# Optimization experiments

Measured on AMD Instinct MI355X. Metric: run time of the kernel, lower is better.

## Reference

```python
import jax, jax.numpy as jnp
import numpy as np

D_MODEL = 1024
D_STATE = 16
LN_EPS = 1e-5


def setup_inputs() -> dict:
    key = jax.random.key(0)
    ks = jax.random.split(key, 10)
    B, T = 8, 4096
    s = 1.0 / np.sqrt(D_MODEL)
    inp = {
        "x": jax.random.normal(ks[0], (B, T, D_MODEL), jnp.float32),
        "h0": jnp.zeros((B, D_STATE), jnp.float32),
        "mask": jnp.ones((B, T), jnp.float32),
        # params
        "A_diag": -jnp.abs(jax.random.normal(ks[1], (D_STATE,), jnp.float32) * 0.01),
        "W_delta": jax.random.uniform(ks[2], (D_STATE, D_MODEL), jnp.float32, -s, s),
        "W_B": jax.random.uniform(ks[3], (D_STATE, D_MODEL), jnp.float32, -s, s),
        "W_C": jax.random.uniform(ks[4], (D_STATE, D_MODEL), jnp.float32, -s, s),
        "W_out": jax.random.uniform(ks[5], (D_MODEL, D_STATE), jnp.float32, -1/np.sqrt(D_STATE), 1/np.sqrt(D_STATE)),
        "D": jnp.ones((D_MODEL,), jnp.float32),
        "W_gate": jax.random.uniform(ks[6], (D_MODEL, D_MODEL), jnp.float32, -s, s),
        "b_gate": jax.random.uniform(ks[7], (D_MODEL,), jnp.float32, -s, s),
        "ln_w": jnp.ones((D_MODEL,), jnp.float32),
        "ln_b": jnp.zeros((D_MODEL,), jnp.float32),
    }
    return inp


def _layernorm(x, w, b):
    mu = jnp.mean(x, axis=-1, keepdims=True)
    var = jnp.var(x, axis=-1, keepdims=True)
    return (x - mu) * jax.lax.rsqrt(var + LN_EPS) * w + b


def reference(x, h0, mask, A_diag, W_delta, W_B, W_C, W_out, D, W_gate, b_gate, ln_w, ln_b):
    # Per-step projections depend only on x_t -> vectorize over T up front.
    gate = jax.nn.sigmoid(_layernorm(jnp.einsum('btd,ed->bte', x, W_gate) + b_gate, ln_w, ln_b))
    xg = gate * x                                        # [B,T,d_model]
    delta = jax.nn.softplus(jnp.einsum('btd,sd->bts', xg, W_delta))
    Bt = jnp.einsum('btd,sd->bts', xg, W_B)              # [B,T,d_state]
    Ct = jnp.einsum('btd,sd->bts', xg, W_C)
    A_bar = jnp.exp(delta * A_diag)                      # [B,T,d_state]
    m = mask[..., None]                                  # [B,T,1]

    def step(h, inputs):
        a_t, b_t, m_t = inputs                           # [B,ds],[B,ds],[B,1]
        h_cand = jnp.tanh(a_t * h + b_t)
        h_new = h_cand * m_t + h * (1.0 - m_t)
        return h_new, h_new

    # scan over time: move T to leading axis
    h_final, hs = jax.lax.scan(
        step, h0,
        (jnp.swapaxes(A_bar, 0, 1), jnp.swapaxes(Bt, 0, 1), jnp.swapaxes(m, 0, 1)))
    hs = jnp.swapaxes(hs, 0, 1)                          # [B,T,d_state]
    s = Ct * hs
    y = jnp.einsum('bts,ds->btd', s, W_out) + D * x      # [B,T,d_model]
    return (y, h_final)
```

## Files before the change

kernel.cpp:

```cpp
#include <hip/hip_runtime.h>
#include <hip/hip_bf16.h>
#include <cstdint>

#define M_TOK   32768
#define LNEPS   1e-5f
#define TWO_LOG2E 2.8853900817779268f

typedef float  f32x4 __attribute__((ext_vector_type(4)));
typedef short  s16x8 __attribute__((ext_vector_type(8)));

__device__ __forceinline__ unsigned short f2b(float v) {
  return __builtin_bit_cast(unsigned short, __float2bfloat16(v));
}
__device__ __forceinline__ float b2f(unsigned short u) {
  return __bfloat162float(__builtin_bit_cast(__hip_bfloat16, u));
}

__device__ __forceinline__ void async_cp16(const void* g, void* l) {
  using gp = const __attribute__((address_space(1))) char*;
  using lp = __attribute__((address_space(3))) char*;
  __builtin_amdgcn_global_load_lds((gp)(uint64_t)g,
                                   (lp)(uint32_t)(uint64_t)l, 16, 0, 0);
}

__global__ __launch_bounds__(256) void k_convert(
    const float* __restrict__ x, const float* __restrict__ wg,
    const float* __restrict__ wd, const float* __restrict__ wb,
    const float* __restrict__ wc,
    unsigned short* __restrict__ Xb, unsigned short* __restrict__ Wgb,
    unsigned short* __restrict__ Wcat) {
  int i = blockIdx.x * 256 + threadIdx.x;
  const float* src;
  unsigned short* dst;
  if (i < 8388608) {
    src = x + (size_t)i * 4; dst = Xb + (size_t)i * 4;
  } else if (i < 8650752) {
    int j = i - 8388608;
    src = wg + (size_t)j * 4; dst = Wgb + (size_t)j * 4;
  } else {
    int j = i - 8650752;
    int e = j * 4;
    if (e < 16384)       src = wd + e;
    else if (e < 32768)  src = wb + (e - 16384);
    else                 src = wc + (e - 32768);
    dst = Wcat + e;
  }
  float4 v = *(const float4*)src;
  ushort4 o;
  o.x = f2b(v.x); o.y = f2b(v.y); o.z = f2b(v.z); o.w = f2b(v.w);
  *(ushort4*)dst = o;
}

__global__ __launch_bounds__(256, 2) void k_gemm_gate(
    const unsigned short* __restrict__ A,
    const unsigned short* __restrict__ Bm,
    unsigned short* __restrict__ C) {
  __shared__ unsigned short As[128 * 32];
  __shared__ unsigned short Bs[128 * 32];
  const int tid  = threadIdx.x;
  const int wave = tid >> 6, lane = tid & 63;
  const int wr = wave >> 1, wc = wave & 1;
  const int lrow = lane & 15, lq = lane >> 4;
  const int lin  = blockIdx.y * gridDim.x + blockIdx.x;
  const int unit = (lin & 7) * 256 + (lin >> 3);
  const int m0 = (unit >> 3) * 128;
  const int n0 = (unit & 7) * 128;
  const int crow  = tid >> 2;
  const int ccol  = (tid & 3) * 8;

  f32x4 acc[4][4];
#pragma unroll
  for (int i = 0; i < 4; i++)
#pragma unroll
    for (int j = 0; j < 4; j++) acc[i][j] = (f32x4){0.f, 0.f, 0.f, 0.f};

  for (int k0 = 0; k0 < 1024; k0 += 32) {
    async_cp16(A + (size_t)(m0 + crow) * 1024 + k0 + ccol,
               (void*)(As + (wave * 64) * 8));
    async_cp16(A + (size_t)(m0 + crow + 64) * 1024 + k0 + ccol,
               (void*)(As + (256 + wave * 64) * 8));
    async_cp16(Bm + (size_t)(n0 + crow) * 1024 + k0 + ccol,
               (void*)(Bs + (wave * 64) * 8));
    async_cp16(Bm + (size_t)(n0 + crow + 64) * 1024 + k0 + ccol,
               (void*)(Bs + (256 + wave * 64) * 8));
    __syncthreads();

    s16x8 af[4], bfr[4];
#pragma unroll
    for (int i = 0; i < 4; i++)
      af[i] = *(const s16x8*)(As + (wr * 64 + i * 16 + lrow) * 32 + lq * 8);
#pragma unroll
    for (int j = 0; j < 4; j++)
      bfr[j] = *(const s16x8*)(Bs + (wc * 64 + j * 16 + lrow) * 32 + lq * 8);
#pragma unroll
    for (int i = 0; i < 4; i++)
#pragma unroll
      for (int j = 0; j < 4; j++)
        acc[i][j] = __builtin_amdgcn_mfma_f32_16x16x32_bf16(
            af[i], bfr[j], acc[i][j], 0, 0, 0);
    __syncthreads();
  }

#pragma unroll
  for (int i = 0; i < 4; i++)
#pragma unroll
    for (int j = 0; j < 4; j++)
#pragma unroll
      for (int r = 0; r < 4; r++) {
        int row = m0 + wr * 64 + i * 16 + lq * 4 + r;
        int col = n0 + wc * 64 + j * 16 + lrow;
        C[(size_t)row * 1024 + col] = f2b(acc[i][j][r]);
      }
}

__global__ __launch_bounds__(256) void k_lngate(
    const unsigned short* Gin, const float* __restrict__ x,
    const float* __restrict__ bg, const float* __restrict__ lnw,
    const float* __restrict__ lnb, unsigned short* XG) {
  __shared__ float red[8];
  const int t = threadIdx.x;
  const size_t r = blockIdx.x;
  const int e = t * 4;

  ushort4 g4 = *(const ushort4*)(Gin + r * 1024 + e);
  float4 bg4 = *(const float4*)(bg + e);
  float v0 = b2f(g4.x) + bg4.x;
  float v1 = b2f(g4.y) + bg4.y;
  float v2 = b2f(g4.z) + bg4.z;
  float v3 = b2f(g4.w) + bg4.w;

  float s  = v0 + v1 + v2 + v3;
  float ss = v0 * v0 + v1 * v1 + v2 * v2 + v3 * v3;
#pragma unroll
  for (int off = 32; off >= 1; off >>= 1) {
    s  += __shfl_xor(s, off, 64);
    ss += __shfl_xor(ss, off, 64);
  }
  if ((t & 63) == 0) { red[t >> 6] = s; red[4 + (t >> 6)] = ss; }
  __syncthreads();
  float tot = red[0] + red[1] + red[2] + red[3];
  float tss = red[4] + red[5] + red[6] + red[7];
  float mu  = tot * (1.0f / 1024.0f);
  float var = tss * (1.0f / 1024.0f) - mu * mu;
  float rs  = rsqrtf(var + LNEPS);

  float4 xv = *(const float4*)(x + r * 1024 + e);
  float4 w4 = *(const float4*)(lnw + e);
  float4 b4 = *(const float4*)(lnb + e);
  float u0 = (v0 - mu) * rs * w4.x + b4.x;
  float u1 = (v1 - mu) * rs * w4.y + b4.y;
  float u2 = (v2 - mu) * rs * w4.z + b4.z;
  float u3 = (v3 - mu) * rs * w4.w + b4.w;
  float g0 = 1.0f / (1.0f + __expf(-u0));
  float g1 = 1.0f / (1.0f + __expf(-u1));
  float g2 = 1.0f / (1.0f + __expf(-u2));
  float g3 = 1.0f / (1.0f + __expf(-u3));
  ushort4 o;
  o.x = f2b(g0 * xv.x); o.y = f2b(g1 * xv.y);
  o.z = f2b(g2 * xv.z); o.w = f2b(g3 * xv.w);
  *(ushort4*)(XG + r * 1024 + e) = o;
}

__global__ __launch_bounds__(256) void k_proj(
    const unsigned short* __restrict__ XG, const unsigned short* __restrict__ Wcat,
    const float* __restrict__ A_diag,
    float* __restrict__ UV, float* __restrict__ Ct, int* __restrict__ flags) {
  __shared__ unsigned short As[64 * 32];
  __shared__ unsigned short Bs[48 * 32];
  const int tid  = threadIdx.x;
  const int wave = tid >> 6, lane = tid & 63;
  const int lrow = lane & 15, lq = lane >> 4;
  const int r0 = blockIdx.x * 64;
  const int crow = tid >> 2, ccol = (tid & 3) * 8;

  if (blockIdx.x == 0 && tid < 8)
    __hip_atomic_store(&flags[tid], 0, __ATOMIC_RELAXED,
                       __HIP_MEMORY_SCOPE_AGENT);

  f32x4 acc[3];
#pragma unroll
  for (int j = 0; j < 3; j++) acc[j] = (f32x4){0.f, 0.f, 0.f, 0.f};

  for (int k0 = 0; k0 < 1024; k0 += 32) {
    uint4 av = *(const uint4*)(XG + (size_t)(r0 + crow) * 1024 + k0 + ccol);
    uint4 bv;
    if (tid < 192) bv = *(const uint4*)(Wcat + (size_t)crow * 1024 + k0 + ccol);
    __syncthreads();
    *(uint4*)(As + crow * 32 + ccol) = av;
    if (tid < 192) *(uint4*)(Bs + crow * 32 + ccol) = bv;
    __syncthreads();
    s16x8 af = *(const s16x8*)(As + (wave * 16 + lrow) * 32 + lq * 8);
#pragma unroll
    for (int j = 0; j < 3; j++) {
      s16x8 bf8 = *(const s16x8*)(Bs + (j * 16 + lrow) * 32 + lq * 8);
      acc[j] = __builtin_amdgcn_mfma_f32_16x16x32_bf16(af, bf8, acc[j], 0, 0, 0);
    }
  }

  float ad = A_diag[lrow];
#pragma unroll
  for (int r = 0; r < 4; r++) {
    int row = r0 + wave * 16 + lq * 4 + r;
    float z  = acc[0][r];
    float sp = fmaxf(z, 0.0f) + log1pf(__expf(-fabsf(z)));
    float A2 = __expf(sp * ad) * TWO_LOG2E;
    float B2 = acc[1][r] * TWO_LOG2E;
    float2 o;
    o.x = A2 + B2;
    o.y = -2.0f * A2;
    *(float2*)(UV + (size_t)row * 32 + lrow * 2) = o;
    Ct[(size_t)row * 16 + lrow] = acc[2][r];
  }
}

#define TC 128
#define NCH (4096 / TC)
#define NOUT 512

__device__ __forceinline__ void load16(float2 (&P)[16], const float* uvb,
                                       int j, int lane) {
#pragma unroll
  for (int i = 0; i < 16; ++i)
    P[i] = *(const float2*)(uvb + ((j * 16 + i) * 16 + lane) * 2);
}
__device__ __forceinline__ void fast16(float2 (&P)[16], float& r, float& h,
                                       float* hhb, int j, int lane) {
#pragma unroll
  for (int i = 0; i < 16; ++i) {
    float w = fmaf(P[i].y, r, P[i].x);
    float e = __builtin_amdgcn_exp2f(w);
    r = __builtin_amdgcn_rcpf(e + 1.0f);
    h = fmaf(-2.0f, r, 1.0f);
    hhb[(j * 16 + i) * 16 + lane] = h;
  }
}
__device__ __forceinline__ void slow16(float2 (&P)[16], float& h,
                                       const float* mb, float* hhb,
                                       int j, int lane) {
#pragma unroll
  for (int i = 0; i < 16; ++i) {
    float v  = P[i].y, u = P[i].x;
    float A2 = -0.5f * v;
    float B2 = fmaf(0.5f, v, u);
    float w  = fmaf(A2, h, B2);
    float e  = __builtin_amdgcn_exp2f(w);
    float rr = __builtin_amdgcn_rcpf(e + 1.0f);
    float th = fmaf(-2.0f, rr, 1.0f);
    float m  = mb[j * 16 + i];
    h = fmaf(m, th - h, h);
    hhb[(j * 16 + i) * 16 + lane] = h;
  }
}

__global__ __launch_bounds__(512, 6) void k_scan_out(
    const float* __restrict__ UV, const float* __restrict__ mask,
    const float* __restrict__ h0, float* __restrict__ hs,
    float* __restrict__ hfin,
    const float* __restrict__ Ct, const float* __restrict__ x,
    const float* __restrict__ Wout, const float* __restrict__ Dd,
    float* __restrict__ y, int* __restrict__ flags) {
  __shared__ float uvL[2][TC * 32];
  __shared__ float hhL[2][TC * 16];
  __shared__ float mskL[2][TC];

  const int tid = threadIdx.x;

  if (blockIdx.x >= 8) {
    const int o    = blockIdx.x - 8;
    const int wv   = tid >> 6;
    const int lane = tid & 63;
    const int d0   = wv * 128 + lane * 2;
    const int b0   = o >> 7;
    const int b1   = b0 + 4;
    const int j0   = o & 127;

    float wa[16], wb[16];
#pragma unroll
    for (int q = 0; q < 4; q++) {
      *(float4*)&wa[q * 4] = *(const float4*)(Wout + (size_t)d0 * 16 + q * 4);
      *(float4*)&wb[q * 4] = *(const float4*)(Wout + (size_t)(d0 + 1) * 16 + q * 4);
    }
    float2 D2 = *(const float2*)(Dd + d0);

    for (int c = 0; c < NCH; ++c) {
      size_t r0 = (size_t)b0 * 4096 + (size_t)c * TC + j0;
      size_t r1 = (size_t)b1 * 4096 + (size_t)c * TC + j0;
      int spins = 0;
      for (;;) {
        int f = 0;
        if (lane == 0) {
          int fa = __hip_atomic_load(&flags[b0], __ATOMIC_RELAXED,
                                     __HIP_MEMORY_SCOPE_AGENT);
          int fb = __hip_atomic_load(&flags[b1], __ATOMIC_RELAXED,
                                     __HIP_MEMORY_SCOPE_AGENT);
          f = (fa < fb) ? fa : fb;
        }
        f = __shfl(f, 0);
        if (f > c || spins > (1 << 18)) break;
        ++spins;
        __builtin_amdgcn_s_sleep(32);
      }
      float cv0 = Ct[r0 * 16 + (lane & 15)];
      float cv1 = Ct[r1 * 16 + (lane & 15)];
      float hv0 = __hip_atomic_load(&hs[r0 * 16 + (lane & 15)],
                                    __ATOMIC_RELAXED, __HIP_MEMORY_SCOPE_AGENT);
      float hv1 = __hip_atomic_load(&hs[r1 * 16 + (lane & 15)],
                                    __ATOMIC_RELAXED, __HIP_MEMORY_SCOPE_AGENT);
      float2 x20 = *(const float2*)(x + r0 * 1024 + d0);
      float2 x21 = *(const float2*)(x + r1 * 1024 + d0);
      float sv0 = cv0 * hv0;
      float sv1 = cv1 * hv1;
      float a0x = D2.x * x20.x, a0y = D2.y * x20.y;
      float a1x = D2.x * x21.x, a1y = D2.y * x21.y;
#pragma unroll
      for (int s = 0; s < 16; s++) {
        float s0 = __shfl(sv0, s);
        float s1 = __shfl(sv1, s);
        a0x = fmaf(wa[s], s0, a0x);
        a0y = fmaf(wb[s], s0, a0y);
        a1x = fmaf(wa[s], s1, a1x);
        a1y = fmaf(wb[s], s1, a1y);
      }
      float2 o0; o0.x = a0x; o0.y = a0y;
      float2 o1; o1.x = a1x; o1.y = a1y;
      *(float2*)(y + r0 * 1024 + d0) = o0;
      *(float2*)(y + r1 * 1024 + d0) = o1;
    }
    return;
  }

  const int b   = blockIdx.x;
  const float* pm = mask + (size_t)b * 4096;
  const size_t uvbase = (size_t)b * 4096 * 32;
  const size_t hsbase = (size_t)b * 4096 * 16;

  if (tid < 64) __builtin_amdgcn_s_setprio(3);

  float h = 0.f, r = 0.f;
  if (tid < 16) {
    h = h0[b * 16 + tid];
    r = 0.5f - 0.5f * h;
  }

  if (tid >= 64) {
    int pt = tid - 64;
    const uint4* src = (const uint4*)(UV + uvbase);
    for (int i = pt; i < TC * 8; i += 448) ((uint4*)uvL[0])[i] = src[i];
    if (tid < 128) {
      int l = tid - 64;
      mskL[0][l]      = pm[l];
      mskL[0][l + 64] = pm[l + 64];
    }
  }
  __syncthreads();

  for (int c = 0; c < NCH; ++c) {
    if (c >= 2 && tid == 511) {
      __hip_atomic_store(&flags[b], c - 1, __ATOMIC_RELAXED,
                         __HIP_MEMORY_SCOPE_AGENT);
    }
    const int p = c & 1;
    if (tid < 64) {
      const int lane = tid;
      float mv0 = mskL[p][2 * lane], mv1 = mskL[p][2 * lane + 1];
      bool on = (mv0 == 1.0f) && (mv1 == 1.0f);
      bool allones = (__ballot(on) == 0xFFFFFFFFFFFFFFFFull);
      if (lane < 16) {
        const float* uvb = uvL[p];
        float* hhb = hhL[p];
        float2 Pa[16], Pb[16];
        load16(Pa, uvb, 0, lane);
        if (allones) {
#pragma unroll
          for (int j = 0; j < 8; j += 2) {
            load16(Pb, uvb, j + 1, lane);
            fast16(Pa, r, h, hhb, j, lane);
            if (j + 2 < 8) load16(Pa, uvb, j + 2, lane);
            fast16(Pb, r, h, hhb, j + 1, lane);
          }
        } else {
#pragma unroll
          for (int j = 0; j < 8; j += 2) {
            load16(Pb, uvb, j + 1, lane);
            slow16(Pa, h, mskL[p], hhb, j, lane);
            if (j + 2 < 8) load16(Pa, uvb, j + 2, lane);
            slow16(Pb, h, mskL[p], hhb, j + 1, lane);
          }
          r = 0.5f - 0.5f * h;
        }
      }
    } else {
      int pt = tid - 64;
      if (c + 1 < NCH) {
        const uint4* src =
            (const uint4*)(UV + uvbase + (size_t)(c + 1) * TC * 32);
        uint4* dst = (uint4*)uvL[(c + 1) & 1];
        for (int i = pt; i < TC * 8; i += 448) dst[i] = src[i];
        if (tid < 128) {
          int l = tid - 64;
          mskL[(c + 1) & 1][l]      = pm[(c + 1) * TC + l];
          mskL[(c + 1) & 1][l + 64] = pm[(c + 1) * TC + l + 64];
        }
      }
      if (c > 0) {
        const unsigned long long* s2 = (const unsigned long long*)hhL[(c - 1) & 1];
        unsigned long long* d2 =
            (unsigned long long*)(hs + hsbase + (size_t)(c - 1) * TC * 16);
        for (int i = pt; i < TC * 8; i += 448)
          __hip_atomic_store(&d2[i], s2[i], __ATOMIC_RELAXED,
                             __HIP_MEMORY_SCOPE_AGENT);
      }
    }
    __syncthreads();
  }

  {
    const unsigned long long* s2 = (const unsigned long long*)hhL[(NCH - 1) & 1];
    unsigned long long* d2 =
        (unsigned long long*)(hs + hsbase + (size_t)(NCH - 1) * TC * 16);
    for (int i = tid; i < TC * 8; i += 512)
      __hip_atomic_store(&d2[i], s2[i], __ATOMIC_RELAXED,
                         __HIP_MEMORY_SCOPE_AGENT);
  }
  __syncthreads();
  if (tid == 511) {
    __hip_atomic_store(&flags[b], NCH, __ATOMIC_RELAXED,
                       __HIP_MEMORY_SCOPE_AGENT);
  }
  if (tid < 16) hfin[b * 16 + tid] = h;
}

extern "C" void kernel_launch(void* const* d_in, const int* in_sizes, int n_in,
                              void* d_out, int out_size, void* d_ws, size_t ws_size,
                              hipStream_t stream) {
  const float* x       = (const float*)d_in[0];
  const float* h0      = (const float*)d_in[1];
  const float* mask    = (const float*)d_in[2];
  const float* A_diag  = (const float*)d_in[3];
  const float* W_delta = (const float*)d_in[4];
  const float* W_B     = (const float*)d_in[5];
  const float* W_C     = (const float*)d_in[6];
  const float* W_out   = (const float*)d_in[7];
  const float* Dd      = (const float*)d_in[8];
  const float* W_gate  = (const float*)d_in[9];
  const float* b_gate  = (const float*)d_in[10];
  const float* ln_w    = (const float*)d_in[11];
  const float* ln_b    = (const float*)d_in[12];

  char* ws = (char*)d_ws;
  unsigned short* Xb   = (unsigned short*)(ws);
  unsigned short* Gb   = (unsigned short*)(ws + 67108864);
  unsigned short* Wgb  = (unsigned short*)(ws + 134217728);
  unsigned short* Wcat = (unsigned short*)(ws + 136314880);
  int* flags = (int*)(ws + 136413184);
  float* UVb = (float*)(ws + 136445952);
  float* Ctb = (float*)(ws + 140640256);
  float* hsb = (float*)(ws + 142737408);

  float* y    = (float*)d_out;
  float* hfin = y + 33554432;

  hipLaunchKernelGGL(k_convert, dim3(33840), dim3(256), 0, stream,
                     x, W_gate, W_delta, W_B, W_C, Xb, Wgb, Wcat);
  hipLaunchKernelGGL(k_gemm_gate, dim3(256, 8), dim3(256), 0, stream, Xb, Wgb, Gb);
  hipLaunchKernelGGL(k_lngate, dim3(32768), dim3(256), 0, stream,
                     Gb, x, b_gate, ln_w, ln_b, Gb);
  hipLaunchKernelGGL(k_proj, dim3(512), dim3(256), 0, stream,
                     Gb, Wcat, A_diag, UVb, Ctb, flags);
  hipLaunchKernelGGL(k_scan_out, dim3(8 + NOUT), dim3(512), 0, stream,
                     UVb, mask, h0, hsb, hfin, Ctb, x, W_out, Dd, y, flags);
}
```

Baseline: 500.6 us.

## Fuse layernorm-gate and state projections into the scan/output persistent kernel

Removes the separate layernorm-gate and projection kernels. Their work now runs inside the worker blocks of the scan/output kernel, which compute the gated activations and the delta/B/C projections per row with a lookahead of four chunks. Readiness counters let the scan blocks spin until each chunk's UV data has been produced. C values stay in shared memory rather than global memory. This saves two launches and a round trip of the gated activations through global memory, but the projection is now done with scalar FMAs and wave reductions instead of MFMA, and more spin-wait synchronisation is added.

```diff
diff --git a/kernel.cpp b/kernel.cpp
--- a/kernel.cpp
+++ b/kernel.cpp
@@ -8,6 +8,7 @@
 
 typedef float  f32x4 __attribute__((ext_vector_type(4)));
 typedef short  s16x8 __attribute__((ext_vector_type(8)));
+typedef unsigned long long ull;
 
 __device__ __forceinline__ unsigned short f2b(float v) {
   return __builtin_bit_cast(unsigned short, __float2bfloat16(v));
@@ -28,8 +29,15 @@
     const float* __restrict__ wd, const float* __restrict__ wb,
     const float* __restrict__ wc,
     unsigned short* __restrict__ Xb, unsigned short* __restrict__ Wgb,
-    unsigned short* __restrict__ Wcat) {
+    unsigned short* __restrict__ Wcat, int* __restrict__ sync_arr) {
   int i = blockIdx.x * 256 + threadIdx.x;
+  if (blockIdx.x == 0) {
+    __hip_atomic_store(&sync_arr[threadIdx.x], 0, __ATOMIC_RELAXED,
+                       __HIP_MEMORY_SCOPE_AGENT);
+    if (threadIdx.x < 8)
+      __hip_atomic_store(&sync_arr[256 + threadIdx.x], 0, __ATOMIC_RELAXED,
+                         __HIP_MEMORY_SCOPE_AGENT);
+  }
   const float* src;
   unsigned short* dst;
   if (i < 8388608) {
@@ -113,109 +121,10 @@
       }
 }
 
-__global__ __launch_bounds__(256) void k_lngate(
-    const unsigned short* Gin, const float* __restrict__ x,
-    const float* __restrict__ bg, const float* __restrict__ lnw,
-    const float* __restrict__ lnb, unsigned short* XG) {
-  __shared__ float red[8];
-  const int t = threadIdx.x;
-  const size_t r = blockIdx.x;
-  const int e = t * 4;
-
-  ushort4 g4 = *(const ushort4*)(Gin + r * 1024 + e);
-  float4 bg4 = *(const float4*)(bg + e);
-  float v0 = b2f(g4.x) + bg4.x;
-  float v1 = b2f(g4.y) + bg4.y;
-  float v2 = b2f(g4.z) + bg4.z;
-  float v3 = b2f(g4.w) + bg4.w;
-
-  float s  = v0 + v1 + v2 + v3;
-  float ss = v0 * v0 + v1 * v1 + v2 * v2 + v3 * v3;
-#pragma unroll
-  for (int off = 32; off >= 1; off >>= 1) {
-    s  += __shfl_xor(s, off, 64);
-    ss += __shfl_xor(ss, off, 64);
-  }
-  if ((t & 63) == 0) { red[t >> 6] = s; red[4 + (t >> 6)] = ss; }
-  __syncthreads();
-  float tot = red[0] + red[1] + red[2] + red[3];
-  float tss = red[4] + red[5] + red[6] + red[7];
-  float mu  = tot * (1.0f / 1024.0f);
-  float var = tss * (1.0f / 1024.0f) - mu * mu;
-  float rs  = rsqrtf(var + LNEPS);
-
-  float4 xv = *(const float4*)(x + r * 1024 + e);
-  float4 w4 = *(const float4*)(lnw + e);
-  float4 b4 = *(const float4*)(lnb + e);
-  float u0 = (v0 - mu) * rs * w4.x + b4.x;
-  float u1 = (v1 - mu) * rs * w4.y + b4.y;
-  float u2 = (v2 - mu) * rs * w4.z + b4.z;
-  float u3 = (v3 - mu) * rs * w4.w + b4.w;
-  float g0 = 1.0f / (1.0f + __expf(-u0));
-  float g1 = 1.0f / (1.0f + __expf(-u1));
-  float g2 = 1.0f / (1.0f + __expf(-u2));
-  float g3 = 1.0f / (1.0f + __expf(-u3));
-  ushort4 o;
-  o.x = f2b(g0 * xv.x); o.y = f2b(g1 * xv.y);
-  o.z = f2b(g2 * xv.z); o.w = f2b(g3 * xv.w);
-  *(ushort4*)(XG + r * 1024 + e) = o;
-}
-
-__global__ __launch_bounds__(256) void k_proj(
-    const unsigned short* __restrict__ XG, const unsigned short* __restrict__ Wcat,
-    const float* __restrict__ A_diag,
-    float* __restrict__ UV, float* __restrict__ Ct, int* __restrict__ flags) {
-  __shared__ unsigned short As[64 * 32];
-  __shared__ unsigned short Bs[48 * 32];
-  const int tid  = threadIdx.x;
-  const int wave = tid >> 6, lane = tid & 63;
-  const int lrow = lane & 15, lq = lane >> 4;
-  const int r0 = blockIdx.x * 64;
-  const int crow = tid >> 2, ccol = (tid & 3) * 8;
-
-  if (blockIdx.x == 0 && tid < 8)
-    __hip_atomic_store(&flags[tid], 0, __ATOMIC_RELAXED,
-                       __HIP_MEMORY_SCOPE_AGENT);
-
-  f32x4 acc[3];
-#pragma unroll
-  for (int j = 0; j < 3; j++) acc[j] = (f32x4){0.f, 0.f, 0.f, 0.f};
-
-  for (int k0 = 0; k0 < 1024; k0 += 32) {
-    uint4 av = *(const uint4*)(XG + (size_t)(r0 + crow) * 1024 + k0 + ccol);
-    uint4 bv;
-    if (tid < 192) bv = *(const uint4*)(Wcat + (size_t)crow * 1024 + k0 + ccol);
-    __syncthreads();
-    *(uint4*)(As + crow * 32 + ccol) = av;
-    if (tid < 192) *(uint4*)(Bs + crow * 32 + ccol) = bv;
-    __syncthreads();
-    s16x8 af = *(const s16x8*)(As + (wave * 16 + lrow) * 32 + lq * 8);
-#pragma unroll
-    for (int j = 0; j < 3; j++) {
-      s16x8 bf8 = *(const s16x8*)(Bs + (j * 16 + lrow) * 32 + lq * 8);
-      acc[j] = __builtin_amdgcn_mfma_f32_16x16x32_bf16(af, bf8, acc[j], 0, 0, 0);
-    }
-  }
-
-  float ad = A_diag[lrow];
-#pragma unroll
-  for (int r = 0; r < 4; r++) {
-    int row = r0 + wave * 16 + lq * 4 + r;
-    float z  = acc[0][r];
-    float sp = fmaxf(z, 0.0f) + log1pf(__expf(-fabsf(z)));
-    float A2 = __expf(sp * ad) * TWO_LOG2E;
-    float B2 = acc[1][r] * TWO_LOG2E;
-    float2 o;
-    o.x = A2 + B2;
-    o.y = -2.0f * A2;
-    *(float2*)(UV + (size_t)row * 32 + lrow * 2) = o;
-    Ct[(size_t)row * 16 + lrow] = acc[2][r];
-  }
-}
-
 #define TC 128
 #define NCH (4096 / TC)
-#define NOUT 512
+#define NWRK 512
+#define LOOKA 4
 
 __device__ __forceinline__ void load16(float2 (&P)[16], const float* uvb,
                                        int j, int lane) {
@@ -251,38 +160,134 @@
     hhb[(j * 16 + i) * 16 + lane] = h;
   }
 }
-
-__global__ __launch_bounds__(512, 6) void k_scan_out(
-    const float* __restrict__ UV, const float* __restrict__ mask,
+__device__ __forceinline__ float red64(float v) {
+#pragma unroll
+  for (int off = 32; off >= 1; off >>= 1) v += __shfl_xor(v, off, 64);
+  return v;
+}
+
+__global__ __launch_bounds__(512, 6) void k_fused(
+    float* __restrict__ UV, const float* __restrict__ mask,
     const float* __restrict__ h0, float* __restrict__ hs,
     float* __restrict__ hfin,
-    const float* __restrict__ Ct, const float* __restrict__ x,
+    const float* __restrict__ x,
     const float* __restrict__ Wout, const float* __restrict__ Dd,
-    float* __restrict__ y, int* __restrict__ flags) {
+    float* __restrict__ y, int* __restrict__ sync_arr,
+    const unsigned short* __restrict__ Gb, const float* __restrict__ bg,
+    const float* __restrict__ lnw, const float* __restrict__ lnb,
+    const unsigned short* __restrict__ Wcat, const float* __restrict__ A_diag) {
   __shared__ float uvL[2][TC * 32];
   __shared__ float hhL[2][TC * 16];
   __shared__ float mskL[2][TC];
+  __shared__ float ctL[8][2][16];
 
   const int tid = threadIdx.x;
+  int* flags = sync_arr;
+  int* rdy   = sync_arr + 8;
 
   if (blockIdx.x >= 8) {
     const int o    = blockIdx.x - 8;
     const int wv   = tid >> 6;
     const int lane = tid & 63;
-    const int d0   = wv * 128 + lane * 2;
     const int b0   = o >> 7;
     const int b1   = b0 + 4;
     const int j0   = o & 127;
-
-    float wa[16], wb[16];
+    const int prow = wv >> 2;
+    const int wir  = wv & 3;
+    const int c16  = lane * 16;
+    const int bb   = prow ? b1 : b0;
+
+    float bgv[16], lwv[16], lbv[16], adv[4];
 #pragma unroll
     for (int q = 0; q < 4; q++) {
-      *(float4*)&wa[q * 4] = *(const float4*)(Wout + (size_t)d0 * 16 + q * 4);
-      *(float4*)&wb[q * 4] = *(const float4*)(Wout + (size_t)(d0 + 1) * 16 + q * 4);
+      *(float4*)&bgv[q * 4] = *(const float4*)(bg  + c16 + q * 4);
+      *(float4*)&lwv[q * 4] = *(const float4*)(lnw + c16 + q * 4);
+      *(float4*)&lbv[q * 4] = *(const float4*)(lnb + c16 + q * 4);
+      adv[q] = A_diag[wir + 4 * q];
+    }
+    const int d0 = wv * 128 + lane * 2;
+    float wa[16], wbv[16];
+#pragma unroll
+    for (int q = 0; q < 4; q++) {
+      *(float4*)&wa[q * 4]  = *(const float4*)(Wout + (size_t)d0 * 16 + q * 4);
+      *(float4*)&wbv[q * 4] = *(const float4*)(Wout + (size_t)(d0 + 1) * 16 + q * 4);
     }
     float2 D2 = *(const float2*)(Dd + d0);
 
-    for (int c = 0; c < NCH; ++c) {
+    for (int c = -LOOKA; c < NCH; ++c) {
+      const int kp = c + LOOKA;
+      if (kp < NCH) {
+        const size_t grow = (size_t)bb * 4096 + (size_t)kp * TC + j0;
+        const unsigned short* gp = Gb + grow * 1024 + c16;
+        s16x8 gA = *(const s16x8*)gp;
+        s16x8 gB = *(const s16x8*)(gp + 8);
+        float v[16];
+#pragma unroll
+        for (int i = 0; i < 8; i++) {
+          v[i]     = b2f((unsigned short)gA[i]) + bgv[i];
+          v[8 + i] = b2f((unsigned short)gB[i]) + bgv[8 + i];
+        }
+        float s = 0.f, ss = 0.f;
+#pragma unroll
+        for (int i = 0; i < 16; i++) { s += v[i]; ss += v[i] * v[i]; }
+        s = red64(s); ss = red64(ss);
+        float mu  = s * (1.0f / 1024.0f);
+        float var = ss * (1.0f / 1024.0f) - mu * mu;
+        float rs  = rsqrtf(var + LNEPS);
+        float xg[16];
+#pragma unroll
+        for (int q = 0; q < 4; q++) {
+          float4 x4 = *(const float4*)(x + grow * 1024 + c16 + q * 4);
+          float xv4[4] = {x4.x, x4.y, x4.z, x4.w};
+#pragma unroll
+          for (int i2 = 0; i2 < 4; i2++) {
+            int i = q * 4 + i2;
+            float u = (v[i] - mu) * rs * lwv[i] + lbv[i];
+            float g = 1.0f / (1.0f + __expf(-u));
+            xg[i] = g * xv4[i2];
+          }
+        }
+#pragma unroll
+        for (int k4 = 0; k4 < 4; k4++) {
+          const int s0 = wir + 4 * k4;
+          const unsigned short* wd = Wcat + (size_t)s0 * 1024 + c16;
+          float zD = 0.f, zB = 0.f, zC = 0.f;
+          {
+            s16x8 a0 = *(const s16x8*)wd;
+            s16x8 a1 = *(const s16x8*)(wd + 8);
+            s16x8 b0v = *(const s16x8*)(wd + 16 * 1024);
+            s16x8 b1v = *(const s16x8*)(wd + 16 * 1024 + 8);
+            s16x8 c0v = *(const s16x8*)(wd + 32 * 1024);
+            s16x8 c1v = *(const s16x8*)(wd + 32 * 1024 + 8);
+#pragma unroll
+            for (int i = 0; i < 8; i++) {
+              zD = fmaf(xg[i],     b2f((unsigned short)a0[i]), zD);
+              zD = fmaf(xg[8 + i], b2f((unsigned short)a1[i]), zD);
+              zB = fmaf(xg[i],     b2f((unsigned short)b0v[i]), zB);
+              zB = fmaf(xg[8 + i], b2f((unsigned short)b1v[i]), zB);
+              zC = fmaf(xg[i],     b2f((unsigned short)c0v[i]), zC);
+              zC = fmaf(xg[8 + i], b2f((unsigned short)c1v[i]), zC);
+            }
+          }
+          zD = red64(zD); zB = red64(zB); zC = red64(zC);
+          float sp = fmaxf(zD, 0.0f) + log1pf(__expf(-fabsf(zD)));
+          float A2 = __expf(sp * adv[k4]) * TWO_LOG2E;
+          float B2 = zB * TWO_LOG2E;
+          if (lane == 0) {
+            float2 uvv; uvv.x = A2 + B2; uvv.y = -2.0f * A2;
+            __hip_atomic_store((ull*)(UV + grow * 32 + s0 * 2),
+                               __builtin_bit_cast(ull, uvv),
+                               __ATOMIC_RELAXED, __HIP_MEMORY_SCOPE_AGENT);
+            ctL[kp & 7][prow][s0] = zC;
+          }
+        }
+        __syncthreads();
+        if (tid == 0) {
+          atomicAdd(&rdy[b0 * 32 + kp], 1);
+          atomicAdd(&rdy[b1 * 32 + kp], 1);
+        }
+      }
+      if (c < 0) continue;
       size_t r0 = (size_t)b0 * 4096 + (size_t)c * TC + j0;
       size_t r1 = (size_t)b1 * 4096 + (size_t)c * TC + j0;
       int spins = 0;
@@ -300,8 +305,8 @@
         ++spins;
         __builtin_amdgcn_s_sleep(32);
       }
-      float cv0 = Ct[r0 * 16 + (lane & 15)];
-      float cv1 = Ct[r1 * 16 + (lane & 15)];
+      float cv0 = ctL[c & 7][0][lane & 15];
+      float cv1 = ctL[c & 7][1][lane & 15];
       float hv0 = __hip_atomic_load(&hs[r0 * 16 + (lane & 15)],
                                     __ATOMIC_RELAXED, __HIP_MEMORY_SCOPE_AGENT);
       float hv1 = __hip_atomic_load(&hs[r1 * 16 + (lane & 15)],
@@ -313,13 +318,13 @@
       float a0x = D2.x * x20.x, a0y = D2.y * x20.y;
       float a1x = D2.x * x21.x, a1y = D2.y * x21.y;
 #pragma unroll
-      for (int s = 0; s < 16; s++) {
-        float s0 = __shfl(sv0, s);
-        float s1 = __shfl(sv1, s);
-        a0x = fmaf(wa[s], s0, a0x);
-        a0y = fmaf(wb[s], s0, a0y);
-        a1x = fmaf(wa[s], s1, a1x);
-        a1y = fmaf(wb[s], s1, a1y);
+      for (int sq = 0; sq < 16; sq++) {
+        float s0v = __shfl(sv0, sq);
+        float s1v = __shfl(sv1, sq);
+        a0x = fmaf(wa[sq], s0v, a0x);
+        a0y = fmaf(wbv[sq], s0v, a0y);
+        a1x = fmaf(wa[sq], s1v, a1x);
+        a1y = fmaf(wbv[sq], s1v, a1y);
       }
       float2 o0; o0.x = a0x; o0.y = a0y;
       float2 o1; o1.x = a1x; o1.y = a1y;
@@ -343,9 +348,23 @@
   }
 
   if (tid >= 64) {
+    int spins = 0;
+    for (;;) {
+      int f = 0;
+      if ((tid & 63) == 0)
+        f = __hip_atomic_load(&rdy[b * 32 + 0], __ATOMIC_RELAXED,
+                              __HIP_MEMORY_SCOPE_AGENT);
+      f = __shfl(f, 0);
+      if (f >= 128 || spins > (1 << 18)) break;
+      ++spins;
+      __builtin_amdgcn_s_sleep(16);
+    }
     int pt = tid - 64;
-    const uint4* src = (const uint4*)(UV + uvbase);
-    for (int i = pt; i < TC * 8; i += 448) ((uint4*)uvL[0])[i] = src[i];
+    const ull* src = (const ull*)(UV + uvbase);
+    ull* dst = (ull*)uvL[0];
+    for (int i = pt; i < TC * 16; i += 448)
+      dst[i] = __hip_atomic_load(&src[i], __ATOMIC_RELAXED,
+                                 __HIP_MEMORY_SCOPE_AGENT);
     if (tid < 128) {
       int l = tid - 64;
       mskL[0][l]      = pm[l];
@@ -392,10 +411,22 @@
     } else {
       int pt = tid - 64;
       if (c + 1 < NCH) {
-        const uint4* src =
-            (const uint4*)(UV + uvbase + (size_t)(c + 1) * TC * 32);
-        uint4* dst = (uint4*)uvL[(c + 1) & 1];
-        for (int i = pt; i < TC * 8; i += 448) dst[i] = src[i];
+        int spins = 0;
+        for (;;) {
+          int f = 0;
+          if ((tid & 63) == 0)
+            f = __hip_atomic_load(&rdy[b * 32 + c + 1], __ATOMIC_RELAXED,
+                                  __HIP_MEMORY_SCOPE_AGENT);
+          f = __shfl(f, 0);
+          if (f >= 128 || spins > (1 << 18)) break;
+          ++spins;
+          __builtin_amdgcn_s_sleep(16);
+        }
+        const ull* src = (const ull*)(UV + uvbase + (size_t)(c + 1) * TC * 32);
+        ull* dst = (ull*)uvL[(c + 1) & 1];
+        for (int i = pt; i < TC * 16; i += 448)
+          dst[i] = __hip_atomic_load(&src[i], __ATOMIC_RELAXED,
+                                     __HIP_MEMORY_SCOPE_AGENT);
         if (tid < 128) {
           int l = tid - 64;
           mskL[(c + 1) & 1][l]      = pm[(c + 1) * TC + l];
@@ -403,9 +434,8 @@
         }
       }
       if (c > 0) {
-        const unsigned long long* s2 = (const unsigned long long*)hhL[(c - 1) & 1];
-        unsigned long long* d2 =
-            (unsigned long long*)(hs + hsbase + (size_t)(c - 1) * TC * 16);
+        const ull* s2 = (const ull*)hhL[(c - 1) & 1];
+        ull* d2 = (ull*)(hs + hsbase + (size_t)(c - 1) * TC * 16);
         for (int i = pt; i < TC * 8; i += 448)
           __hip_atomic_store(&d2[i], s2[i], __ATOMIC_RELAXED,
                              __HIP_MEMORY_SCOPE_AGENT);
@@ -415,9 +445,8 @@
   }
 
   {
-    const unsigned long long* s2 = (const unsigned long long*)hhL[(NCH - 1) & 1];
-    unsigned long long* d2 =
-        (unsigned long long*)(hs + hsbase + (size_t)(NCH - 1) * TC * 16);
+    const ull* s2 = (const ull*)hhL[(NCH - 1) & 1];
+    ull* d2 = (ull*)(hs + hsbase + (size_t)(NCH - 1) * TC * 16);
     for (int i = tid; i < TC * 8; i += 512)
       __hip_atomic_store(&d2[i], s2[i], __ATOMIC_RELAXED,
                          __HIP_MEMORY_SCOPE_AGENT);
@@ -452,21 +481,17 @@
   unsigned short* Gb   = (unsigned short*)(ws + 67108864);
   unsigned short* Wgb  = (unsigned short*)(ws + 134217728);
   unsigned short* Wcat = (unsigned short*)(ws + 136314880);
-  int* flags = (int*)(ws + 136413184);
+  int* sync_arr = (int*)(ws + 136413184);
   float* UVb = (float*)(ws + 136445952);
-  float* Ctb = (float*)(ws + 140640256);
   float* hsb = (float*)(ws + 142737408);
 
   float* y    = (float*)d_out;
   float* hfin = y + 33554432;
 
   hipLaunchKernelGGL(k_convert, dim3(33840), dim3(256), 0, stream,
-                     x, W_gate, W_delta, W_B, W_C, Xb, Wgb, Wcat);
+                     x, W_gate, W_delta, W_B, W_C, Xb, Wgb, Wcat, sync_arr);
   hipLaunchKernelGGL(k_gemm_gate, dim3(256, 8), dim3(256), 0, stream, Xb, Wgb, Gb);
-  hipLaunchKernelGGL(k_lngate, dim3(32768), dim3(256), 0, stream,
-                     Gb, x, b_gate, ln_w, ln_b, Gb);
-  hipLaunchKernelGGL(k_proj, dim3(512), dim3(256), 0, stream,
-                     Gb, Wcat, A_diag, UVb, Ctb, flags);
-  hipLaunchKernelGGL(k_scan_out, dim3(8 + NOUT), dim3(512), 0, stream,
-                     UVb, mask, h0, hsb, hfin, Ctb, x, W_out, Dd, y, flags);
-}
+  hipLaunchKernelGGL(k_fused, dim3(8 + NWRK), dim3(512), 0, stream,
+                     UVb, mask, h0, hsb, hfin, x, W_out, Dd, y, sync_arr,
+                     Gb, b_gate, ln_w, ln_b, Wcat, A_diag);
+}
```

New measurement: 1.349 ms. 169% more time.

## Fuse LayerNorm-gate into the state projection GEMM prologue

Applied to the files above, without the earlier changes.

Removes the separate LayerNorm+sigmoid gating kernel and computes per-row mean/rstd inside the projection kernel, then applies the gate and multiplies by x while staging the A tile into shared memory. This avoids writing and rereading the gated bf16 activation buffer and one kernel launch. In exchange the projection kernel reads the gate output twice and loads fp32 x plus LN parameters in its inner loop, with only 512 blocks to hide that latency.

```diff
diff --git a/kernel.cpp b/kernel.cpp
--- a/kernel.cpp
+++ b/kernel.cpp
@@ -8,12 +8,18 @@
 
 typedef float  f32x4 __attribute__((ext_vector_type(4)));
 typedef short  s16x8 __attribute__((ext_vector_type(8)));
+typedef unsigned long long ull;
 
 __device__ __forceinline__ unsigned short f2b(float v) {
   return __builtin_bit_cast(unsigned short, __float2bfloat16(v));
 }
 __device__ __forceinline__ float b2f(unsigned short u) {
   return __bfloat162float(__builtin_bit_cast(__hip_bfloat16, u));
+}
+__device__ __forceinline__ float red64(float v) {
+#pragma unroll
+  for (int off = 32; off >= 1; off >>= 1) v += __shfl_xor(v, off, 64);
+  return v;
 }
 
 __device__ __forceinline__ void async_cp16(const void* g, void* l) {
@@ -113,60 +119,17 @@
       }
 }
 
-__global__ __launch_bounds__(256) void k_lngate(
-    const unsigned short* Gin, const float* __restrict__ x,
-    const float* __restrict__ bg, const float* __restrict__ lnw,
-    const float* __restrict__ lnb, unsigned short* XG) {
-  __shared__ float red[8];
-  const int t = threadIdx.x;
-  const size_t r = blockIdx.x;
-  const int e = t * 4;
-
-  ushort4 g4 = *(const ushort4*)(Gin + r * 1024 + e);
-  float4 bg4 = *(const float4*)(bg + e);
-  float v0 = b2f(g4.x) + bg4.x;
-  float v1 = b2f(g4.y) + bg4.y;
-  float v2 = b2f(g4.z) + bg4.z;
-  float v3 = b2f(g4.w) + bg4.w;
-
-  float s  = v0 + v1 + v2 + v3;
-  float ss = v0 * v0 + v1 * v1 + v2 * v2 + v3 * v3;
-#pragma unroll
-  for (int off = 32; off >= 1; off >>= 1) {
-    s  += __shfl_xor(s, off, 64);
-    ss += __shfl_xor(ss, off, 64);
-  }
-  if ((t & 63) == 0) { red[t >> 6] = s; red[4 + (t >> 6)] = ss; }
-  __syncthreads();
-  float tot = red[0] + red[1] + red[2] + red[3];
-  float tss = red[4] + red[5] + red[6] + red[7];
-  float mu  = tot * (1.0f / 1024.0f);
-  float var = tss * (1.0f / 1024.0f) - mu * mu;
-  float rs  = rsqrtf(var + LNEPS);
-
-  float4 xv = *(const float4*)(x + r * 1024 + e);
-  float4 w4 = *(const float4*)(lnw + e);
-  float4 b4 = *(const float4*)(lnb + e);
-  float u0 = (v0 - mu) * rs * w4.x + b4.x;
-  float u1 = (v1 - mu) * rs * w4.y + b4.y;
-  float u2 = (v2 - mu) * rs * w4.z + b4.z;
-  float u3 = (v3 - mu) * rs * w4.w + b4.w;
-  float g0 = 1.0f / (1.0f + __expf(-u0));
-  float g1 = 1.0f / (1.0f + __expf(-u1));
-  float g2 = 1.0f / (1.0f + __expf(-u2));
-  float g3 = 1.0f / (1.0f + __expf(-u3));
-  ushort4 o;
-  o.x = f2b(g0 * xv.x); o.y = f2b(g1 * xv.y);
-  o.z = f2b(g2 * xv.z); o.w = f2b(g3 * xv.w);
-  *(ushort4*)(XG + r * 1024 + e) = o;
-}
-
-__global__ __launch_bounds__(256) void k_proj(
-    const unsigned short* __restrict__ XG, const unsigned short* __restrict__ Wcat,
+__global__ __launch_bounds__(256) void k_lnproj(
+    const unsigned short* __restrict__ G,
+    const float* __restrict__ x,
+    const float* __restrict__ bgp, const float* __restrict__ lnw,
+    const float* __restrict__ lnb,
+    const unsigned short* __restrict__ Wcat,
     const float* __restrict__ A_diag,
     float* __restrict__ UV, float* __restrict__ Ct, int* __restrict__ flags) {
   __shared__ unsigned short As[64 * 32];
   __shared__ unsigned short Bs[48 * 32];
+  __shared__ float muL[64], rsL[64];
   const int tid  = threadIdx.x;
   const int wave = tid >> 6, lane = tid & 63;
   const int lrow = lane & 15, lq = lane >> 4;
@@ -177,16 +140,65 @@
     __hip_atomic_store(&flags[tid], 0, __ATOMIC_RELAXED,
                        __HIP_MEMORY_SCOPE_AGENT);
 
+  {
+    float bga[8], bgb[8];
+    *(float4*)&bga[0] = *(const float4*)(bgp + lane * 8);
+    *(float4*)&bga[4] = *(const float4*)(bgp + lane * 8 + 4);
+    *(float4*)&bgb[0] = *(const float4*)(bgp + 512 + lane * 8);
+    *(float4*)&bgb[4] = *(const float4*)(bgp + 512 + lane * 8 + 4);
+    for (int rr = 0; rr < 16; ++rr) {
+      const int row = wave * 16 + rr;
+      const unsigned short* gp = G + (size_t)(r0 + row) * 1024;
+      s16x8 ga = *(const s16x8*)(gp + lane * 8);
+      s16x8 gb = *(const s16x8*)(gp + 512 + lane * 8);
+      float s = 0.f, ss = 0.f;
+#pragma unroll
+      for (int i = 0; i < 8; i++) {
+        float va = b2f((unsigned short)ga[i]) + bga[i];
+        float vb = b2f((unsigned short)gb[i]) + bgb[i];
+        s  += va + vb;
+        ss += va * va + vb * vb;
+      }
+      s = red64(s); ss = red64(ss);
+      if (lane == 0) {
+        float mu  = s * (1.0f / 1024.0f);
+        float var = ss * (1.0f / 1024.0f) - mu * mu;
+        muL[row] = mu;
+        rsL[row] = rsqrtf(var + LNEPS);
+      }
+    }
+  }
+  __syncthreads();
+  const float mu = muL[crow];
+  const float rs = rsL[crow];
+
   f32x4 acc[3];
 #pragma unroll
   for (int j = 0; j < 3; j++) acc[j] = (f32x4){0.f, 0.f, 0.f, 0.f};
 
   for (int k0 = 0; k0 < 1024; k0 += 32) {
-    uint4 av = *(const uint4*)(XG + (size_t)(r0 + crow) * 1024 + k0 + ccol);
+    s16x8 gv = *(const s16x8*)(G + (size_t)(r0 + crow) * 1024 + k0 + ccol);
+    float xs[8], bgs[8], lws[8], lbs[8];
+    *(float4*)&xs[0]  = *(const float4*)(x   + (size_t)(r0 + crow) * 1024 + k0 + ccol);
+    *(float4*)&xs[4]  = *(const float4*)(x   + (size_t)(r0 + crow) * 1024 + k0 + ccol + 4);
+    *(float4*)&bgs[0] = *(const float4*)(bgp + k0 + ccol);
+    *(float4*)&bgs[4] = *(const float4*)(bgp + k0 + ccol + 4);
+    *(float4*)&lws[0] = *(const float4*)(lnw + k0 + ccol);
+    *(float4*)&lws[4] = *(const float4*)(lnw + k0 + ccol + 4);
+    *(float4*)&lbs[0] = *(const float4*)(lnb + k0 + ccol);
+    *(float4*)&lbs[4] = *(const float4*)(lnb + k0 + ccol + 4);
     uint4 bv;
     if (tid < 192) bv = *(const uint4*)(Wcat + (size_t)crow * 1024 + k0 + ccol);
     __syncthreads();
-    *(uint4*)(As + crow * 32 + ccol) = av;
+    s16x8 ov;
+#pragma unroll
+    for (int i = 0; i < 8; i++) {
+      float v = b2f((unsigned short)gv[i]) + bgs[i];
+      float u = (v - mu) * rs * lws[i] + lbs[i];
+      float g = 1.0f / (1.0f + __expf(-u));
+      ov[i] = (short)f2b(g * xs[i]);
+    }
+    *(s16x8*)(As + crow * 32 + ccol) = ov;
     if (tid < 192) *(uint4*)(Bs + crow * 32 + ccol) = bv;
     __syncthreads();
     s16x8 af = *(const s16x8*)(As + (wave * 16 + lrow) * 32 + lq * 8);
@@ -403,9 +415,8 @@
         }
       }
       if (c > 0) {
-        const unsigned long long* s2 = (const unsigned long long*)hhL[(c - 1) & 1];
-        unsigned long long* d2 =
-            (unsigned long long*)(hs + hsbase + (size_t)(c - 1) * TC * 16);
+        const ull* s2 = (const ull*)hhL[(c - 1) & 1];
+        ull* d2 = (ull*)(hs + hsbase + (size_t)(c - 1) * TC * 16);
         for (int i = pt; i < TC * 8; i += 448)
           __hip_atomic_store(&d2[i], s2[i], __ATOMIC_RELAXED,
                              __HIP_MEMORY_SCOPE_AGENT);
@@ -415,9 +426,8 @@
   }
 
   {
-    const unsigned long long* s2 = (const unsigned long long*)hhL[(NCH - 1) & 1];
-    unsigned long long* d2 =
-        (unsigned long long*)(hs + hsbase + (size_t)(NCH - 1) * TC * 16);
+    const ull* s2 = (const ull*)hhL[(NCH - 1) & 1];
+    ull* d2 = (ull*)(hs + hsbase + (size_t)(NCH - 1) * TC * 16);
     for (int i = tid; i < TC * 8; i += 512)
       __hip_atomic_store(&d2[i], s2[i], __ATOMIC_RELAXED,
                          __HIP_MEMORY_SCOPE_AGENT);
@@ -463,10 +473,8 @@
   hipLaunchKernelGGL(k_convert, dim3(33840), dim3(256), 0, stream,
                      x, W_gate, W_delta, W_B, W_C, Xb, Wgb, Wcat);
   hipLaunchKernelGGL(k_gemm_gate, dim3(256, 8), dim3(256), 0, stream, Xb, Wgb, Gb);
-  hipLaunchKernelGGL(k_lngate, dim3(32768), dim3(256), 0, stream,
-                     Gb, x, b_gate, ln_w, ln_b, Gb);
-  hipLaunchKernelGGL(k_proj, dim3(512), dim3(256), 0, stream,
-                     Gb, Wcat, A_diag, UVb, Ctb, flags);
+  hipLaunchKernelGGL(k_lnproj, dim3(512), dim3(256), 0, stream,
+                     Gb, x, b_gate, ln_w, ln_b, Wcat, A_diag, UVb, Ctb, flags);
   hipLaunchKernelGGL(k_scan_out, dim3(8 + NOUT), dim3(512), 0, stream,
                      UVb, mask, h0, hsb, hfin, Ctb, x, W_out, Dd, y, flags);
 }
```

Result: no change. 497.9 us (-0.6%).
